# Performance work log

Hardware: AMD Instinct MI355X
Metric: run time of the kernel (lower is better)

## Reference

```python
import jax, jax.numpy as jnp
import numpy as np

ALPHA = 2.0  # snntorch ATan surrogate default (irrelevant for fwd-only)


def _spike(x):
    return (x > 0).astype(x.dtype)


def setup_inputs() -> dict:
    key = jax.random.key(0)
    ks = jax.random.split(key, 7)
    B, T, H, O = 2048, 120, 512, 2
    sample_rate = 40.0
    x = jax.random.normal(ks[0], (B, T), dtype=jnp.float32)
    # fc1: [H, 1], fc2: [O, H] (torch Linear weight layout), gaussian init near 1/sample_rate scale
    W1 = (1.0 / sample_rate) + (0.5 / sample_rate) * jax.random.normal(ks[1], (H, 1), dtype=jnp.float32)
    W2 = (1.0 / (sample_rate * H)) + (0.5 / (sample_rate * H)) * jax.random.normal(ks[2], (O, H), dtype=jnp.float32)
    W2 = W2 * H  # keep output currents at a useful magnitude
    beta_h = 0.8 + 0.19 * jax.random.uniform(ks[3], (H,), dtype=jnp.float32)
    thr_h = 1.0 + 0.1 * jax.random.uniform(ks[4], (H,), dtype=jnp.float32)
    beta_o = 0.8 + 0.19 * jax.random.uniform(ks[5], (O,), dtype=jnp.float32)
    thr_o = 1.0 + 0.1 * jax.random.uniform(ks[6], (O,), dtype=jnp.float32)
    return {"x": x, "W1": W1, "W2": W2, "beta_h": beta_h, "thr_h": thr_h,
            "beta_o": beta_o, "thr_o": thr_o}


def reference(x, W1, W2, beta_h, thr_h, beta_o, thr_o):
    B = x.shape[0]
    H, O = W1.shape[0], W2.shape[0]
    bh = jnp.clip(beta_h, 0.0, 1.0)
    bo = jnp.clip(beta_o, 0.0, 1.0)
    w1 = W1[:, 0]  # [H]; fc1 on scalar input is an outer product

    def step(carry, x_t):
        mem1, mem2 = carry
        cur1 = x_t[:, None] * w1[None, :]              # [B, H]
        mem1 = bh * mem1 + cur1
        spk1 = _spike(mem1 - thr_h)
        mem1 = mem1 * (1.0 - spk1)                      # zero reset, no delay
        cur2 = spk1 @ W2.T                              # [B, O]
        mem2 = bo * mem2 + cur2
        spk2 = _spike(mem2 - thr_o)
        mem2 = mem2 * (1.0 - spk2)
        return (mem1, mem2), (spk1, mem1, spk2, mem2)

    init = (jnp.zeros((B, H), x.dtype), jnp.zeros((B, O), x.dtype))
    xT = x.T  # [T, B] so scan walks time steps
    _, (spk1_rec, mem1_rec, spk2_rec, mem2_rec) = jax.lax.scan(step, init, xT)
    hidden_spike_count = spk1_rec.sum()
    output_spike_count = spk2_rec.sum()
    return spk1_rec, mem1_rec, spk2_rec, mem2_rec, hidden_spike_count, output_spike_count
```

## Files before the change

kernel.cpp:

```cpp
#include <hip/hip_runtime.h>

#define T_STEPS 120
#define BATCH   2048
#define HID     512
#define OUTN    2

#define SPK1_OFF 0LL
#define MEM1_OFF 125829120LL
#define SPK2_OFF 251658240LL
#define MEM2_OFF 252149760LL
#define CNT_OFF  252641280LL

typedef float f32x4 __attribute__((ext_vector_type(4)));

__global__ void zero_counts_kernel(float* cnts) {
    cnts[0] = 0.0f;
    cnts[1] = 0.0f;
}

__global__ __launch_bounds__(128) void snn_fwd_kernel(
    const float* __restrict__ x,
    const float* __restrict__ W1,
    const float* __restrict__ W2,
    const float* __restrict__ beta_h,
    const float* __restrict__ thr_h,
    const float* __restrict__ beta_o,
    const float* __restrict__ thr_o,
    float* __restrict__ spk1_rec,
    float* __restrict__ mem1_rec,
    float* __restrict__ spk2_rec,
    float* __restrict__ mem2_rec,
    float* __restrict__ cnts)
{
    const int tid  = threadIdx.x;
    const int b    = blockIdx.x;
    const int wid  = tid >> 6;
    const int lane = tid & 63;

    __shared__ float xs[T_STEPS];
    __shared__ float red[T_STEPS][2][2];
    __shared__ float redc[2];

    if (tid < T_STEPS) {
        ((f32x4*)red)[tid] = (f32x4)0.0f;
        xs[tid] = x[(size_t)b * T_STEPS + tid];
    }

    const f32x4 w1v  = ((const f32x4*)W1)[tid];
    f32x4 bhv        = ((const f32x4*)beta_h)[tid];
    const f32x4 thv  = ((const f32x4*)thr_h)[tid];
    const f32x4 w20v = ((const f32x4*)W2)[tid];
    const f32x4 w21v = ((const f32x4*)(W2 + HID))[tid];
    bhv.x = fminf(fmaxf(bhv.x, 0.0f), 1.0f);
    bhv.y = fminf(fmaxf(bhv.y, 0.0f), 1.0f);
    bhv.z = fminf(fmaxf(bhv.z, 0.0f), 1.0f);
    bhv.w = fminf(fmaxf(bhv.w, 0.0f), 1.0f);

    float m0 = 0.0f, m1 = 0.0f, m2 = 0.0f, m3 = 0.0f;
    int hc = 0;

    __syncthreads();

    const size_t off1    = (size_t)b * HID + (size_t)tid * 4;
    const size_t stride1 = (size_t)BATCH * HID;
    float* sp = spk1_rec + off1;
    float* mp = mem1_rec + off1;

    #pragma unroll 4
    for (int t = 0; t < T_STEPS; ++t) {
        const float xt = xs[t];
        m0 = __fadd_rn(__fmul_rn(bhv.x, m0), __fmul_rn(xt, w1v.x));
        m1 = __fadd_rn(__fmul_rn(bhv.y, m1), __fmul_rn(xt, w1v.y));
        m2 = __fadd_rn(__fmul_rn(bhv.z, m2), __fmul_rn(xt, w1v.z));
        m3 = __fadd_rn(__fmul_rn(bhv.w, m3), __fmul_rn(xt, w1v.w));

        const bool f0 = m0 > thv.x;
        const bool f1 = m1 > thv.y;
        const bool f2 = m2 > thv.z;
        const bool f3 = m3 > thv.w;
        const float s0 = f0 ? 1.0f : 0.0f;
        const float s1 = f1 ? 1.0f : 0.0f;
        const float s2 = f2 ? 1.0f : 0.0f;
        const float s3 = f3 ? 1.0f : 0.0f;
        m0 = f0 ? 0.0f : m0;
        m1 = f1 ? 0.0f : m1;
        m2 = f2 ? 0.0f : m2;
        m3 = f3 ? 0.0f : m3;
        hc += (int)f0 + (int)f1 + (int)f2 + (int)f3;

        f32x4 sv; sv.x = s0; sv.y = s1; sv.z = s2; sv.w = s3;
        f32x4 mv; mv.x = m0; mv.y = m1; mv.z = m2; mv.w = m3;
        __builtin_nontemporal_store(sv, (f32x4*)sp);
        __builtin_nontemporal_store(mv, (f32x4*)mp);
        sp += stride1;
        mp += stride1;

        if (__ballot(f0 | f1 | f2 | f3) != 0ULL) {
            float c0 = s0 * w20v.x + s1 * w20v.y + s2 * w20v.z + s3 * w20v.w;
            float c1 = s0 * w21v.x + s1 * w21v.y + s2 * w21v.z + s3 * w21v.w;
            #pragma unroll
            for (int o = 32; o > 0; o >>= 1) {
                c0 += __shfl_down(c0, o, 64);
                c1 += __shfl_down(c1, o, 64);
            }
            if (lane == 0) { red[t][wid][0] = c0; red[t][wid][1] = c1; }
        }
    }

    float fc = (float)hc;
    #pragma unroll
    for (int o = 32; o > 0; o >>= 1) fc += __shfl_down(fc, o, 64);
    if (lane == 0) redc[wid] = fc;

    __syncthreads();

    if (tid == 0) atomicAdd(&cnts[0], redc[0] + redc[1]);

    if (tid < OUTN) {
        const int o = tid;
        const float bo = fminf(fmaxf(beta_o[o], 0.0f), 1.0f);
        const float to = thr_o[o];
        float m = 0.0f;
        int oc = 0;
        const size_t stride2 = (size_t)BATCH * OUTN;
        float* s2p = spk2_rec + (size_t)b * OUTN + o;
        float* m2p = mem2_rec + (size_t)b * OUTN + o;
        #pragma unroll 4
        for (int t = 0; t < T_STEPS; ++t) {
            const float cur = red[t][0][o] + red[t][1][o];
            m = __fadd_rn(__fmul_rn(bo, m), cur);
            const bool f = m > to;
            const float s = f ? 1.0f : 0.0f;
            if (f) { m = 0.0f; oc++; }
            s2p[0] = s;
            m2p[0] = m;
            s2p += stride2;
            m2p += stride2;
        }
        if (oc) atomicAdd(&cnts[1], (float)oc);
    }
}

extern "C" void kernel_launch(void* const* d_in, const int* in_sizes, int n_in,
                              void* d_out, int out_size, void* d_ws, size_t ws_size,
                              hipStream_t stream) {
    const float* x      = (const float*)d_in[0];
    const float* W1     = (const float*)d_in[1];
    const float* W2     = (const float*)d_in[2];
    const float* beta_h = (const float*)d_in[3];
    const float* thr_h  = (const float*)d_in[4];
    const float* beta_o = (const float*)d_in[5];
    const float* thr_o  = (const float*)d_in[6];

    float* out  = (float*)d_out;
    float* spk1 = out + SPK1_OFF;
    float* mem1 = out + MEM1_OFF;
    float* spk2 = out + SPK2_OFF;
    float* mem2 = out + MEM2_OFF;
    float* cnts = out + CNT_OFF;

    zero_counts_kernel<<<1, 1, 0, stream>>>(cnts);

    snn_fwd_kernel<<<BATCH, 128, 0, stream>>>(
        x, W1, W2, beta_h, thr_h, beta_o, thr_o,
        spk1, mem1, spk2, mem2, cnts);
}
```

Baseline: 1.034 ms.

## Map one wavefront per batch row with eight rows per block

Each batch row is now handled by a single 64-lane wavefront that owns eight hidden neurons per lane, and each 512-thread block covers eight rows. Because a row lives in one wavefront, the cross-wave shared-memory reduction and the block barrier before the output-layer recurrence go away, and the hidden spike count is accumulated per wave with atomics. The cost is more registers per thread, more atomics on the count, and a different store pattern in which each wave writes two 1 KB halves of a row per time step. The kernel is bound by output bandwidth, so the gain may be small.

```diff
diff --git a/kernel.cpp b/kernel.cpp
--- a/kernel.cpp
+++ b/kernel.cpp
@@ -4,6 +4,7 @@
 #define BATCH   2048
 #define HID     512
 #define OUTN    2
+#define G_ROWS  8
 
 #define SPK1_OFF 0LL
 #define MEM1_OFF 125829120LL
@@ -12,13 +13,21 @@
 #define CNT_OFF  252641280LL
 
 typedef float f32x4 __attribute__((ext_vector_type(4)));
+typedef float f32x2 __attribute__((ext_vector_type(2)));
 
 __global__ void zero_counts_kernel(float* cnts) {
     cnts[0] = 0.0f;
     cnts[1] = 0.0f;
 }
 
-__global__ __launch_bounds__(128) void snn_fwd_kernel(
+#define HSTEP(mm, bb, ww, tt, ss, ff)                                  \
+    mm = __fadd_rn(__fmul_rn(bb, mm), __fmul_rn(xt, ww));              \
+    const bool  ff = mm > tt;                                          \
+    const float ss = ff ? 1.0f : 0.0f;                                 \
+    mm = ff ? 0.0f : mm;                                               \
+    hc += (int)ff;
+
+__global__ __launch_bounds__(512) void snn_fwd_kernel(
     const float* __restrict__ x,
     const float* __restrict__ W1,
     const float* __restrict__ W2,
@@ -33,109 +42,111 @@
     float* __restrict__ cnts)
 {
     const int tid  = threadIdx.x;
-    const int b    = blockIdx.x;
-    const int wid  = tid >> 6;
+    const int w    = tid >> 6;
     const int lane = tid & 63;
+    const int b    = blockIdx.x * G_ROWS + w;
 
-    __shared__ float xs[T_STEPS];
-    __shared__ float red[T_STEPS][2][2];
-    __shared__ float redc[2];
+    __shared__ float xs[G_ROWS][T_STEPS];
+    __shared__ float red[G_ROWS][T_STEPS][2];
 
-    if (tid < T_STEPS) {
-        ((f32x4*)red)[tid] = (f32x4)0.0f;
-        xs[tid] = x[(size_t)b * T_STEPS + tid];
+    if (lane < 60) {
+        ((f32x2*)xs[w])[lane]  = ((const f32x2*)x)[(size_t)b * (T_STEPS / 2) + lane];
+        ((f32x4*)red[w])[lane] = (f32x4)0.0f;
     }
 
-    const f32x4 w1v  = ((const f32x4*)W1)[tid];
-    f32x4 bhv        = ((const f32x4*)beta_h)[tid];
-    const f32x4 thv  = ((const f32x4*)thr_h)[tid];
-    const f32x4 w20v = ((const f32x4*)W2)[tid];
-    const f32x4 w21v = ((const f32x4*)(W2 + HID))[tid];
-    bhv.x = fminf(fmaxf(bhv.x, 0.0f), 1.0f);
-    bhv.y = fminf(fmaxf(bhv.y, 0.0f), 1.0f);
-    bhv.z = fminf(fmaxf(bhv.z, 0.0f), 1.0f);
-    bhv.w = fminf(fmaxf(bhv.w, 0.0f), 1.0f);
+    const int pA = lane;
+    const int pB = 64 + lane;
+    const f32x4 w1A  = ((const f32x4*)W1)[pA];
+    const f32x4 w1B  = ((const f32x4*)W1)[pB];
+    f32x4 bhA        = ((const f32x4*)beta_h)[pA];
+    f32x4 bhB        = ((const f32x4*)beta_h)[pB];
+    const f32x4 thA  = ((const f32x4*)thr_h)[pA];
+    const f32x4 thB  = ((const f32x4*)thr_h)[pB];
+    const f32x4 w20A = ((const f32x4*)W2)[pA];
+    const f32x4 w20B = ((const f32x4*)W2)[pB];
+    const f32x4 w21A = ((const f32x4*)(W2 + HID))[pA];
+    const f32x4 w21B = ((const f32x4*)(W2 + HID))[pB];
+    bhA.x = fminf(fmaxf(bhA.x, 0.0f), 1.0f);
+    bhA.y = fminf(fmaxf(bhA.y, 0.0f), 1.0f);
+    bhA.z = fminf(fmaxf(bhA.z, 0.0f), 1.0f);
+    bhA.w = fminf(fmaxf(bhA.w, 0.0f), 1.0f);
+    bhB.x = fminf(fmaxf(bhB.x, 0.0f), 1.0f);
+    bhB.y = fminf(fmaxf(bhB.y, 0.0f), 1.0f);
+    bhB.z = fminf(fmaxf(bhB.z, 0.0f), 1.0f);
+    bhB.w = fminf(fmaxf(bhB.w, 0.0f), 1.0f);
 
-    float m0 = 0.0f, m1 = 0.0f, m2 = 0.0f, m3 = 0.0f;
+    float mA0 = 0.f, mA1 = 0.f, mA2 = 0.f, mA3 = 0.f;
+    float mB0 = 0.f, mB1 = 0.f, mB2 = 0.f, mB3 = 0.f;
     int hc = 0;
 
     __syncthreads();
 
-    const size_t off1    = (size_t)b * HID + (size_t)tid * 4;
-    const size_t stride1 = (size_t)BATCH * HID;
-    float* sp = spk1_rec + off1;
-    float* mp = mem1_rec + off1;
+    const size_t st1 = (size_t)BATCH * HID;
+    float* sp = spk1_rec + (size_t)b * HID + (size_t)lane * 4;
+    float* mp = mem1_rec + (size_t)b * HID + (size_t)lane * 4;
 
-    #pragma unroll 4
+    #pragma unroll 2
     for (int t = 0; t < T_STEPS; ++t) {
-        const float xt = xs[t];
-        m0 = __fadd_rn(__fmul_rn(bhv.x, m0), __fmul_rn(xt, w1v.x));
-        m1 = __fadd_rn(__fmul_rn(bhv.y, m1), __fmul_rn(xt, w1v.y));
-        m2 = __fadd_rn(__fmul_rn(bhv.z, m2), __fmul_rn(xt, w1v.z));
-        m3 = __fadd_rn(__fmul_rn(bhv.w, m3), __fmul_rn(xt, w1v.w));
+        const float xt = xs[w][t];
 
-        const bool f0 = m0 > thv.x;
-        const bool f1 = m1 > thv.y;
-        const bool f2 = m2 > thv.z;
-        const bool f3 = m3 > thv.w;
-        const float s0 = f0 ? 1.0f : 0.0f;
-        const float s1 = f1 ? 1.0f : 0.0f;
-        const float s2 = f2 ? 1.0f : 0.0f;
-        const float s3 = f3 ? 1.0f : 0.0f;
-        m0 = f0 ? 0.0f : m0;
-        m1 = f1 ? 0.0f : m1;
-        m2 = f2 ? 0.0f : m2;
-        m3 = f3 ? 0.0f : m3;
-        hc += (int)f0 + (int)f1 + (int)f2 + (int)f3;
+        HSTEP(mA0, bhA.x, w1A.x, thA.x, sA0, fA0)
+        HSTEP(mA1, bhA.y, w1A.y, thA.y, sA1, fA1)
+        HSTEP(mA2, bhA.z, w1A.z, thA.z, sA2, fA2)
+        HSTEP(mA3, bhA.w, w1A.w, thA.w, sA3, fA3)
+        HSTEP(mB0, bhB.x, w1B.x, thB.x, sB0, fB0)
+        HSTEP(mB1, bhB.y, w1B.y, thB.y, sB1, fB1)
+        HSTEP(mB2, bhB.z, w1B.z, thB.z, sB2, fB2)
+        HSTEP(mB3, bhB.w, w1B.w, thB.w, sB3, fB3)
 
-        f32x4 sv; sv.x = s0; sv.y = s1; sv.z = s2; sv.w = s3;
-        f32x4 mv; mv.x = m0; mv.y = m1; mv.z = m2; mv.w = m3;
-        __builtin_nontemporal_store(sv, (f32x4*)sp);
-        __builtin_nontemporal_store(mv, (f32x4*)mp);
-        sp += stride1;
-        mp += stride1;
+        f32x4 sAv; sAv.x = sA0; sAv.y = sA1; sAv.z = sA2; sAv.w = sA3;
+        f32x4 sBv; sBv.x = sB0; sBv.y = sB1; sBv.z = sB2; sBv.w = sB3;
+        f32x4 mAv; mAv.x = mA0; mAv.y = mA1; mAv.z = mA2; mAv.w = mA3;
+        f32x4 mBv; mBv.x = mB0; mBv.y = mB1; mBv.z = mB2; mBv.w = mB3;
+        __builtin_nontemporal_store(sAv, (f32x4*)sp);
+        __builtin_nontemporal_store(sBv, (f32x4*)(sp + 256));
+        __builtin_nontemporal_store(mAv, (f32x4*)mp);
+        __builtin_nontemporal_store(mBv, (f32x4*)(mp + 256));
+        sp += st1;
+        mp += st1;
 
-        if (__ballot(f0 | f1 | f2 | f3) != 0ULL) {
-            float c0 = s0 * w20v.x + s1 * w20v.y + s2 * w20v.z + s3 * w20v.w;
-            float c1 = s0 * w21v.x + s1 * w21v.y + s2 * w21v.z + s3 * w21v.w;
+        if (__ballot(fA0 | fA1 | fA2 | fA3 | fB0 | fB1 | fB2 | fB3) != 0ULL) {
+            float c0 = sA0 * w20A.x + sA1 * w20A.y + sA2 * w20A.z + sA3 * w20A.w
+                     + sB0 * w20B.x + sB1 * w20B.y + sB2 * w20B.z + sB3 * w20B.w;
+            float c1 = sA0 * w21A.x + sA1 * w21A.y + sA2 * w21A.z + sA3 * w21A.w
+                     + sB0 * w21B.x + sB1 * w21B.y + sB2 * w21B.z + sB3 * w21B.w;
             #pragma unroll
             for (int o = 32; o > 0; o >>= 1) {
                 c0 += __shfl_down(c0, o, 64);
                 c1 += __shfl_down(c1, o, 64);
             }
-            if (lane == 0) { red[t][wid][0] = c0; red[t][wid][1] = c1; }
+            if (lane == 0) { red[w][t][0] = c0; red[w][t][1] = c1; }
         }
     }
 
     float fc = (float)hc;
     #pragma unroll
     for (int o = 32; o > 0; o >>= 1) fc += __shfl_down(fc, o, 64);
-    if (lane == 0) redc[wid] = fc;
+    if (lane == 0) atomicAdd(&cnts[0], fc);
 
-    __syncthreads();
-
-    if (tid == 0) atomicAdd(&cnts[0], redc[0] + redc[1]);
-
-    if (tid < OUTN) {
-        const int o = tid;
+    if (lane < OUTN) {
+        const int o = lane;
         const float bo = fminf(fmaxf(beta_o[o], 0.0f), 1.0f);
         const float to = thr_o[o];
         float m = 0.0f;
         int oc = 0;
-        const size_t stride2 = (size_t)BATCH * OUTN;
+        const size_t st2 = (size_t)BATCH * OUTN;
         float* s2p = spk2_rec + (size_t)b * OUTN + o;
         float* m2p = mem2_rec + (size_t)b * OUTN + o;
         #pragma unroll 4
         for (int t = 0; t < T_STEPS; ++t) {
-            const float cur = red[t][0][o] + red[t][1][o];
+            const float cur = red[w][t][o];
             m = __fadd_rn(__fmul_rn(bo, m), cur);
             const bool f = m > to;
-            const float s = f ? 1.0f : 0.0f;
+            s2p[0] = f ? 1.0f : 0.0f;
             if (f) { m = 0.0f; oc++; }
-            s2p[0] = s;
             m2p[0] = m;
-            s2p += stride2;
-            m2p += stride2;
+            s2p += st2;
+            m2p += st2;
         }
         if (oc) atomicAdd(&cnts[1], (float)oc);
     }
@@ -161,7 +172,7 @@
 
     zero_counts_kernel<<<1, 1, 0, stream>>>(cnts);
 
-    snn_fwd_kernel<<<BATCH, 128, 0, stream>>>(
+    snn_fwd_kernel<<<BATCH / G_ROWS, 512, 0, stream>>>(
         x, W1, W2, beta_h, thr_h, beta_o, thr_o,
         spk1, mem1, spk2, mem2, cnts);
 }
```

Measured after the change: 1.008 ms. -2.6%, faster.
